# Kernel tuning notes

Hardware: AMD Instinct MI355X
Metric: run time of the kernel (lower is better)

Reference implementation:

```python
import jax, jax.numpy as jnp
import numpy as np
import math

EMBED_DIM = 1024
NUM_HEADS = 16
PROJ_DIM = 1024
HEAD_DIM = PROJ_DIM // NUM_HEADS  # 64
ALPHA = 0.3  # warmup_steps=0, step_count irrelevant -> alpha_eff = alpha
DIFFUSION_STEPS = 2


def setup_inputs() -> dict:
    key = jax.random.key(0)
    ks = jax.random.split(key, 9)
    B, N, D = 1, 2048, EMBED_DIM
    s_in = 1.0 / math.sqrt(D)
    s_p = 1.0 / math.sqrt(PROJ_DIM)
    return {
        "hidden_states": jax.random.normal(ks[0], (B, N, D), dtype=jnp.float32),
        # Linear weights stored as [in, out] (apply as x @ W + b)
        "Wq": jax.random.normal(ks[1], (D, PROJ_DIM), dtype=jnp.float32) * s_in,
        "bq": jax.random.normal(ks[2], (PROJ_DIM,), dtype=jnp.float32) * s_in,
        "Wk": jax.random.normal(ks[3], (D, PROJ_DIM), dtype=jnp.float32) * s_in,
        "bk": jax.random.normal(ks[4], (PROJ_DIM,), dtype=jnp.float32) * s_in,
        "Wv": jax.random.normal(ks[5], (D, PROJ_DIM), dtype=jnp.float32) * s_in,
        "bv": jax.random.normal(ks[6], (PROJ_DIM,), dtype=jnp.float32) * s_in,
        "Wo": jax.random.normal(ks[7], (PROJ_DIM, D), dtype=jnp.float32) * s_p,
        "bo": jax.random.normal(ks[8], (D,), dtype=jnp.float32) * s_p,
    }


def reference(hidden_states, Wq, bq, Wk, bk, Wv, bv, Wo, bo):
    B, N, D = hidden_states.shape
    H, hd = NUM_HEADS, HEAD_DIM

    def split_heads(x):  # [B, N, P] -> [B, H, N, hd]
        return x.reshape(B, -1, H, hd).transpose(0, 2, 1, 3)

    Q = split_heads(hidden_states @ Wq + bq)
    K = split_heads(hidden_states @ Wk + bk)
    V = split_heads(hidden_states @ Wv + bv)

    # scores: note original uses (sqrt(hd) + 1e-8) denominator here
    scores = jnp.einsum("bhqd,bhkd->bhqk", Q, K) / (math.sqrt(hd) + 1e-8)
    p0 = jax.nn.softmax(scores, axis=-1)

    # key-transition matrix P: exact sqrt(hd) denominator
    sim = jnp.einsum("bhid,bhjd->bhij", K, K) / math.sqrt(hd)
    P = jax.nn.softmax(sim, axis=-1)

    # iterative diffusion, unrolled (early-stop can only fire after the
    # final update when diffusion_steps=2, so output is identical)
    a = ALPHA
    p = p0
    for _ in range(DIFFUSION_STEPS):
        p = (1.0 - a) * p0 + a * jnp.einsum("bhqn,bhnm->bhqm", p, P)

    attn = jnp.einsum("bhqk,bhkd->bhqd", p, V)
    attn = attn.transpose(0, 2, 1, 3).reshape(B, N, PROJ_DIM)
    out = attn @ Wo + bo
    return out, p
```

## Files before the change

### kernel.cpp

```cpp
#include <hip/hip_runtime.h>


typedef __attribute__((ext_vector_type(8))) short bf16x8;
typedef __attribute__((ext_vector_type(4))) short s16x4;
typedef __attribute__((ext_vector_type(4))) float f32x4;

constexpr int N_TOK   = 2048;
constexpr int N_HEADS = 16;
constexpr int HD      = 64;
constexpr int EMB     = 1024;

#define DEVINL __device__ __forceinline__

DEVINL unsigned short f2bf_u(float f) {
  unsigned x = __float_as_uint(f);
  return (unsigned short)((x + 0x7fffu + ((x >> 16) & 1u)) >> 16);
}
DEVINL float bf2f_u(unsigned short h) { return __uint_as_float(((unsigned)h) << 16); }

DEVINL void async16(const void* src, void* dst) {
  __builtin_amdgcn_global_load_lds(
      (const __attribute__((address_space(1))) void*)src,
      (__attribute__((address_space(3))) void*)dst, 16, 0, 0);
}

enum : int { EPI_F32SCALE = 0, EPI_F32BIAS, EPI_BF16, EPI_QKSPLIT, EPI_VSPLIT,
             EPI_DIFF_BF16, EPI_DIFF_F32 };

template<int EPI>
__global__ __launch_bounds__(512, 2)
void gemm256_diff(const unsigned short* __restrict__ Am, int lda, long long sAz,
                  const unsigned short* __restrict__ Bm, int ldb, long long sBz,
                  int K,
                  const unsigned short* __restrict__ P0, int ldp0, long long sPz,
                  void* __restrict__ Cv, int ldc, long long sCz)
{
  __shared__ __align__(16) char smem[2 * 65536];
  const int tid  = threadIdx.x;
  const int lane = tid & 63, wv = tid >> 6;
  const int wr = wv >> 2, wc = wv & 3;
  const int l15 = lane & 15, g = lane >> 4;
  const int z = blockIdx.z;
  const size_t brow = (size_t)blockIdx.y * 256;
  const size_t bcol = (size_t)blockIdx.x * 256;

  const unsigned short* Ab = Am + (size_t)z * (size_t)sAz;
  const unsigned short* Bb = Bm + (size_t)z * (size_t)sBz;
  const int NT = K >> 6;

  const int cbs = (tid & 7) * 16;
  const int r00 = (tid >> 3),       r01 = 64  + (tid >> 3);
  const int r10 = 128 + (tid >> 3), r11 = 192 + (tid >> 3);
  const char* gA00 = (const char*)Ab + ((brow + r00) * (size_t)lda) * 2 + (cbs ^ ((r00 & 7) << 4));
  const char* gA01 = (const char*)Ab + ((brow + r01) * (size_t)lda) * 2 + (cbs ^ ((r01 & 7) << 4));
  const char* gA10 = (const char*)Ab + ((brow + r10) * (size_t)lda) * 2 + (cbs ^ ((r10 & 7) << 4));
  const char* gA11 = (const char*)Ab + ((brow + r11) * (size_t)lda) * 2 + (cbs ^ ((r11 & 7) << 4));
  const char* gB00 = (const char*)Bb + ((bcol + r00) * (size_t)ldb) * 2 + (cbs ^ ((r00 & 7) << 4));
  const char* gB01 = (const char*)Bb + ((bcol + r01) * (size_t)ldb) * 2 + (cbs ^ ((r01 & 7) << 4));
  const char* gB10 = (const char*)Bb + ((bcol + r10) * (size_t)ldb) * 2 + (cbs ^ ((r10 & 7) << 4));
  const char* gB11 = (const char*)Bb + ((bcol + r11) * (size_t)ldb) * 2 + (cbs ^ ((r11 & 7) << 4));

  f32x4 acc[8][4];
  #pragma unroll
  for (int m = 0; m < 8; ++m)
    #pragma unroll
    for (int n = 0; n < 4; ++n) acc[m][n] = f32x4{0.f, 0.f, 0.f, 0.f};

  auto ldA = [&](int cur, int mf, int kk) -> bf16x8 {
    const int row = wr * 128 + mf * 16 + l15;
    const int c = (kk * 64 + g * 16) ^ ((row & 7) << 4);
    return *(const bf16x8*)(smem + cur * 65536 + row * 128 + c);
  };
  auto ldB = [&](int cur, int nf, int kk) -> bf16x8 {
    const int row = wc * 64 + nf * 16 + l15;
    const int c = (kk * 64 + g * 16) ^ ((row & 7) << 4);
    return *(const bf16x8*)(smem + cur * 65536 + 32768 + row * 128 + c);
  };

  {
    char* d0 = smem;
    async16(gA00, d0 +             wv * 1024);
    async16(gA01, d0 +  8192 +     wv * 1024);
    async16(gA10, d0 + 16384 +     wv * 1024);
    async16(gA11, d0 + 24576 +     wv * 1024);
    async16(gB00, d0 + 32768 +     wv * 1024);
    async16(gB01, d0 + 40960 +     wv * 1024);
    async16(gB10, d0 + 49152 +     wv * 1024);
    async16(gB11, d0 + 57344 +     wv * 1024);
    if (NT > 1) {
      char* d1 = smem + 65536 + 32768;
      async16(gB00 + 128, d1 +             wv * 1024);
      async16(gB01 + 128, d1 +  8192 +     wv * 1024);
      async16(gB10 + 128, d1 + 16384 +     wv * 1024);
      async16(gB11 + 128, d1 + 24576 +     wv * 1024);
      asm volatile("s_waitcnt vmcnt(4)" ::: "memory");
    } else {
      asm volatile("s_waitcnt vmcnt(0)" ::: "memory");
    }
    __builtin_amdgcn_sched_barrier(0);
    __builtin_amdgcn_s_barrier();
  }

#define READA(P, Q)                                                       \
    bf16x8 P##00 = ldA(cur, 2*(Q),   0), P##01 = ldA(cur, 2*(Q),   1),    \
           P##10 = ldA(cur, 2*(Q)+1, 0), P##11 = ldA(cur, 2*(Q)+1, 1);

#define MFMA16(P, Q)                                                                        \
    __builtin_amdgcn_s_setprio(1);                                                          \
    acc[2*(Q)+0][0] = __builtin_amdgcn_mfma_f32_16x16x32_bf16(P##00, b00, acc[2*(Q)+0][0], 0, 0, 0); \
    acc[2*(Q)+0][1] = __builtin_amdgcn_mfma_f32_16x16x32_bf16(P##00, b10, acc[2*(Q)+0][1], 0, 0, 0); \
    acc[2*(Q)+0][2] = __builtin_amdgcn_mfma_f32_16x16x32_bf16(P##00, b20, acc[2*(Q)+0][2], 0, 0, 0); \
    acc[2*(Q)+0][3] = __builtin_amdgcn_mfma_f32_16x16x32_bf16(P##00, b30, acc[2*(Q)+0][3], 0, 0, 0); \
    acc[2*(Q)+1][0] = __builtin_amdgcn_mfma_f32_16x16x32_bf16(P##10, b00, acc[2*(Q)+1][0], 0, 0, 0); \
    acc[2*(Q)+1][1] = __builtin_amdgcn_mfma_f32_16x16x32_bf16(P##10, b10, acc[2*(Q)+1][1], 0, 0, 0); \
    acc[2*(Q)+1][2] = __builtin_amdgcn_mfma_f32_16x16x32_bf16(P##10, b20, acc[2*(Q)+1][2], 0, 0, 0); \
    acc[2*(Q)+1][3] = __builtin_amdgcn_mfma_f32_16x16x32_bf16(P##10, b30, acc[2*(Q)+1][3], 0, 0, 0); \
    acc[2*(Q)+0][0] = __builtin_amdgcn_mfma_f32_16x16x32_bf16(P##01, b01, acc[2*(Q)+0][0], 0, 0, 0); \
    acc[2*(Q)+0][1] = __builtin_amdgcn_mfma_f32_16x16x32_bf16(P##01, b11, acc[2*(Q)+0][1], 0, 0, 0); \
    acc[2*(Q)+0][2] = __builtin_amdgcn_mfma_f32_16x16x32_bf16(P##01, b21, acc[2*(Q)+0][2], 0, 0, 0); \
    acc[2*(Q)+0][3] = __builtin_amdgcn_mfma_f32_16x16x32_bf16(P##01, b31, acc[2*(Q)+0][3], 0, 0, 0); \
    acc[2*(Q)+1][0] = __builtin_amdgcn_mfma_f32_16x16x32_bf16(P##11, b01, acc[2*(Q)+1][0], 0, 0, 0); \
    acc[2*(Q)+1][1] = __builtin_amdgcn_mfma_f32_16x16x32_bf16(P##11, b11, acc[2*(Q)+1][1], 0, 0, 0); \
    acc[2*(Q)+1][2] = __builtin_amdgcn_mfma_f32_16x16x32_bf16(P##11, b21, acc[2*(Q)+1][2], 0, 0, 0); \
    acc[2*(Q)+1][3] = __builtin_amdgcn_mfma_f32_16x16x32_bf16(P##11, b31, acc[2*(Q)+1][3], 0, 0, 0); \
    __builtin_amdgcn_s_setprio(0);

#define SB __builtin_amdgcn_sched_barrier(0)

  int cur = 0;
  for (int t = 0; t < NT; ++t, cur ^= 1) {
    const int o = cur ^ 1;
    const size_t ko1 = (size_t)(t + 1) * 128;
    const size_t ko2 = (size_t)(t + 2) * 128;
    bf16x8 b00 = ldB(cur, 0, 0), b01 = ldB(cur, 0, 1);
    bf16x8 b10 = ldB(cur, 1, 0), b11 = ldB(cur, 1, 1);
    bf16x8 b20 = ldB(cur, 2, 0), b21 = ldB(cur, 2, 1);
    bf16x8 b30 = ldB(cur, 3, 0), b31 = ldB(cur, 3, 1);
    READA(f0_, 0)
    READA(f1_, 1)
    if (t + 1 < NT) {
      char* d = smem + o * 65536;
      async16(gA00 + ko1, d +        wv * 1024);
      async16(gA01 + ko1, d + 8192 + wv * 1024);
    }
    asm volatile("s_waitcnt lgkmcnt(4)" ::: "memory");
    SB;
    MFMA16(f0_, 0)
    READA(f2_, 2)
    if (t + 1 < NT) {
      char* d = smem + o * 65536;
      async16(gA10 + ko1, d + 16384 + wv * 1024);
      async16(gA11 + ko1, d + 24576 + wv * 1024);
    }
    asm volatile("s_waitcnt lgkmcnt(4)" ::: "memory");
    SB;
    MFMA16(f1_, 1)
    SB;
    __builtin_amdgcn_s_barrier();
    READA(f3_, 3)
    if (t + 2 < NT) {
      char* d = smem + cur * 65536 + 32768;
      async16(gB00 + ko2, d +        wv * 1024);
      async16(gB01 + ko2, d + 8192 + wv * 1024);
    }
    asm volatile("s_waitcnt lgkmcnt(4)" ::: "memory");
    SB;
    MFMA16(f2_, 2)
    if (t + 2 < NT) {
      char* d = smem + cur * 65536 + 32768 + 16384;
      async16(gB10 + ko2, d +        wv * 1024);
      async16(gB11 + ko2, d + 8192 + wv * 1024);
    }
    asm volatile("s_waitcnt lgkmcnt(0)" ::: "memory");
    SB;
    MFMA16(f3_, 3)
    if (t + 1 < NT) {
      if (t + 2 < NT) asm volatile("s_waitcnt vmcnt(4)" ::: "memory");
      else            asm volatile("s_waitcnt vmcnt(0)" ::: "memory");
      SB;
      __builtin_amdgcn_s_barrier();
    }
  }
#undef MFMA16
#undef READA
#undef SB

  float* Cf = (float*)Cv + (size_t)z * (size_t)sCz;
  unsigned short* Cu = (unsigned short*)Cv + (size_t)z * (size_t)sCz;
  const unsigned short* P0z = P0 + (size_t)z * (size_t)sPz;
  #pragma unroll
  for (int m = 0; m < 8; ++m)
  #pragma unroll
  for (int n = 0; n < 4; ++n)
  #pragma unroll
  for (int j = 0; j < 4; ++j) {
    const size_t R = brow + (size_t)(wr * 128 + m * 16 + g * 4 + j);
    const size_t C = bcol + (size_t)(wc * 64 + n * 16 + l15);
    const float v = acc[m][n][j];
    const float p0v = bf2f_u(P0z[R * (size_t)ldp0 + C]);
    const float r = 0.7f * p0v + 0.3f * v;
    if constexpr (EPI == EPI_DIFF_BF16) Cu[R * ldc + C] = f2bf_u(r);
    else                                Cf[R * ldc + C] = r;
  }
}

template<int BM, int BN, bool AF32, int EPI>
__global__ __launch_bounds__(256)
void gemm_tn(const void* __restrict__ Av, int lda, long long sAz,
             const unsigned short* __restrict__ Bm, int ldb, long long sBz,
             int K, float alpha, const float* __restrict__ bias,
             const unsigned short* __restrict__ P0, int ldp0, long long sPz,
             void* __restrict__ Cv, int ldc, long long sCz)
{
  constexpr int BKk = 64;
  constexpr int WM = BM / 2, WN = BN / 2, MF = WM / 16, NF = WN / 16;
  constexpr int AES = AF32 ? 4 : 2;
  constexpr int ABYTES = BM * BKk * AES, BBYTES = BN * BKk * 2;
  __shared__ __align__(16) char smem[ABYTES + BBYTES];

  const int tid  = threadIdx.x;
  const int lane = tid & 63, wv = tid >> 6;
  const int wr = wv >> 1, wc = wv & 1;
  const int l15 = lane & 15, g = lane >> 4;
  const int z = blockIdx.z;
  const size_t brow = (size_t)blockIdx.y * BM;
  const size_t bcol = (size_t)blockIdx.x * BN;

  const char* Ab = (const char*)Av + (size_t)z * (size_t)sAz * AES;
  const unsigned short* Bb = Bm + (size_t)z * (size_t)sBz;

  f32x4 acc[MF][NF];
  #pragma unroll
  for (int m = 0; m < MF; ++m)
    #pragma unroll
    for (int n = 0; n < NF; ++n)
      acc[m][n] = f32x4{0.f, 0.f, 0.f, 0.f};

  constexpr int EPC_A = AF32 ? 4 : 8;
  constexpr int CPR_A = BKk / EPC_A;
  constexpr int IT_A  = (BM * CPR_A) / 256;
  constexpr int CPR_B = 8;
  constexpr int IT_B  = (BN * CPR_B) / 256;

  for (int k0 = 0; k0 < K; k0 += BKk) {
    #pragma unroll
    for (int i = 0; i < IT_A; ++i) {
      const int c   = i * 256 + wv * 64 + lane;
      const int row = c / CPR_A;
      const int eo  = (c % CPR_A) * EPC_A;
      const char* src = Ab + ((brow + row) * (size_t)lda + (size_t)(k0 + eo)) * AES;
      async16(src, smem + (size_t)(i * 256 + wv * 64) * 16);
    }
    #pragma unroll
    for (int i = 0; i < IT_B; ++i) {
      const int c   = i * 256 + wv * 64 + lane;
      const int row = c / CPR_B;
      const int eo  = (c % CPR_B) * 8;
      const unsigned short* src = Bb + (bcol + row) * (size_t)ldb + (size_t)(k0 + eo);
      async16(src, smem + ABYTES + (size_t)(i * 256 + wv * 64) * 16);
    }
    __syncthreads();
    #pragma unroll
    for (int kk = 0; kk < 2; ++kk) {
      bf16x8 a[MF], b[NF];
      #pragma unroll
      for (int m = 0; m < MF; ++m) {
        const int r = wr * WM + m * 16 + l15;
        if constexpr (!AF32) {
          a[m] = *(const bf16x8*)(smem + ((size_t)r * BKk + kk * 32 + g * 8) * 2);
        } else {
          const float* pa = (const float*)smem + (size_t)r * BKk + kk * 32 + g * 8;
          const f32x4 lo = *(const f32x4*)pa;
          const f32x4 hi = *(const f32x4*)(pa + 4);
          bf16x8 t;
          t[0] = (short)f2bf_u(lo[0]); t[1] = (short)f2bf_u(lo[1]);
          t[2] = (short)f2bf_u(lo[2]); t[3] = (short)f2bf_u(lo[3]);
          t[4] = (short)f2bf_u(hi[0]); t[5] = (short)f2bf_u(hi[1]);
          t[6] = (short)f2bf_u(hi[2]); t[7] = (short)f2bf_u(hi[3]);
          a[m] = t;
        }
      }
      #pragma unroll
      for (int n = 0; n < NF; ++n) {
        const int cc = wc * WN + n * 16 + l15;
        b[n] = *(const bf16x8*)(smem + ABYTES + ((size_t)cc * BKk + kk * 32 + g * 8) * 2);
      }
      #pragma unroll
      for (int m = 0; m < MF; ++m)
        #pragma unroll
        for (int n = 0; n < NF; ++n)
          acc[m][n] = __builtin_amdgcn_mfma_f32_16x16x32_bf16(a[m], b[n], acc[m][n], 0, 0, 0);
    }
    __syncthreads();
  }

  float* Cf = (float*)Cv + (size_t)z * (size_t)sCz;
  unsigned short* Cu = (unsigned short*)Cv + (size_t)z * (size_t)sCz;

  #pragma unroll
  for (int m = 0; m < MF; ++m)
  #pragma unroll
  for (int n = 0; n < NF; ++n)
  #pragma unroll
  for (int j = 0; j < 4; ++j) {
    const size_t R  = brow + (size_t)(wr * WM + m * 16 + g * 4 + j);
    const size_t Cc = bcol + (size_t)(wc * WN + n * 16 + l15);
    const float v = acc[m][n][j];
    if constexpr (EPI == EPI_F32SCALE) {
      Cf[R * ldc + Cc] = v * alpha;
    } else if constexpr (EPI == EPI_F32BIAS) {
      Cf[R * ldc + Cc] = v + bias[Cc];
    } else if constexpr (EPI == EPI_BF16) {
      Cu[R * ldc + Cc] = f2bf_u(v);
    } else if constexpr (EPI == EPI_QKSPLIT) {
      const float t = v + bias[Cc];
      Cu[(Cc >> 6) * ((size_t)N_TOK * HD) + R * HD + (Cc & 63)] = f2bf_u(t);
    } else if constexpr (EPI == EPI_VSPLIT) {
      const float t = v + bias[Cc];
      Cu[(Cc >> 6) * ((size_t)HD * N_TOK) + (Cc & 63) * (size_t)N_TOK + R] = f2bf_u(t);
    } else if constexpr (EPI == EPI_DIFF_BF16) {
      const unsigned short* P0z = P0 + (size_t)z * (size_t)sPz;
      const float p0v = bf2f_u(P0z[R * (size_t)ldp0 + Cc]);
      Cu[R * ldc + Cc] = f2bf_u(0.7f * p0v + 0.3f * v);
    } else if constexpr (EPI == EPI_DIFF_F32) {
      const unsigned short* P0z = P0 + (size_t)z * (size_t)sPz;
      const float p0v = bf2f_u(P0z[R * (size_t)ldp0 + Cc]);
      Cf[R * ldc + Cc] = 0.7f * p0v + 0.3f * v;
    }
  }
  (void)alpha; (void)bias; (void)P0; (void)ldp0;
}

__global__ __launch_bounds__(256)
void row_softmax(const float* __restrict__ S, long long sS,
                 unsigned short* __restrict__ O, long long sO)
{
  __shared__ float red[8];
  const int tid = threadIdx.x;
  const size_t row = blockIdx.x;
  const size_t h = blockIdx.y;
  const f32x4* Sr = (const f32x4*)(S + (size_t)h * sS + row * N_TOK);
  f32x4 v0 = Sr[tid], v1 = Sr[tid + 256];
  float m = fmaxf(fmaxf(fmaxf(v0[0], v0[1]), fmaxf(v0[2], v0[3])),
                  fmaxf(fmaxf(v1[0], v1[1]), fmaxf(v1[2], v1[3])));
  #pragma unroll
  for (int o = 32; o; o >>= 1) m = fmaxf(m, __shfl_xor(m, o));
  if ((tid & 63) == 0) red[tid >> 6] = m;
  __syncthreads();
  m = fmaxf(fmaxf(red[0], red[1]), fmaxf(red[2], red[3]));
  f32x4 e0, e1;
  #pragma unroll
  for (int k = 0; k < 4; ++k) { e0[k] = expf(v0[k] - m); e1[k] = expf(v1[k] - m); }
  float s = e0[0]+e0[1]+e0[2]+e0[3]+e1[0]+e1[1]+e1[2]+e1[3];
  #pragma unroll
  for (int o = 32; o; o >>= 1) s += __shfl_xor(s, o);
  if ((tid & 63) == 0) red[4 + (tid >> 6)] = s;
  __syncthreads();
  s = red[4] + red[5] + red[6] + red[7];
  const float inv = 1.0f / s;
  s16x4 o0, o1;
  #pragma unroll
  for (int k = 0; k < 4; ++k) {
    o0[k] = (short)f2bf_u(e0[k] * inv);
    o1[k] = (short)f2bf_u(e1[k] * inv);
  }
  s16x4* Or = (s16x4*)(O + (size_t)h * sO + row * N_TOK);
  Or[tid] = o0; Or[tid + 256] = o1;
}

__global__ __launch_bounds__(256)
void row_reduce(const float* __restrict__ S, long long sS,
                float* __restrict__ mx, float* __restrict__ is_)
{
  __shared__ float red[8];
  const int tid = threadIdx.x;
  const size_t row = blockIdx.x;
  const size_t h = blockIdx.y;
  const f32x4* Sr = (const f32x4*)(S + (size_t)h * sS + row * N_TOK);
  f32x4 v0 = Sr[tid], v1 = Sr[tid + 256];
  float m = fmaxf(fmaxf(fmaxf(v0[0], v0[1]), fmaxf(v0[2], v0[3])),
                  fmaxf(fmaxf(v1[0], v1[1]), fmaxf(v1[2], v1[3])));
  #pragma unroll
  for (int o = 32; o; o >>= 1) m = fmaxf(m, __shfl_xor(m, o));
  if ((tid & 63) == 0) red[tid >> 6] = m;
  __syncthreads();
  m = fmaxf(fmaxf(red[0], red[1]), fmaxf(red[2], red[3]));
  float s = 0.f;
  #pragma unroll
  for (int k = 0; k < 4; ++k) { s += expf(v0[k] - m); s += expf(v1[k] - m); }
  #pragma unroll
  for (int o = 32; o; o >>= 1) s += __shfl_xor(s, o);
  if ((tid & 63) == 0) red[4 + (tid >> 6)] = s;
  __syncthreads();
  s = red[4] + red[5] + red[6] + red[7];
  if (tid == 0) { mx[h * N_TOK + row] = m; is_[h * N_TOK + row] = 1.0f / s; }
}

__global__ __launch_bounds__(256)
void pt_write(const float* __restrict__ S, long long sS,
              const float* __restrict__ mx, const float* __restrict__ is_,
              unsigned short* __restrict__ PT, long long sP)
{
  const int tid = threadIdx.x;
  const size_t row = blockIdx.x;
  const size_t h = blockIdx.y;
  const f32x4* Sr = (const f32x4*)(S + (size_t)h * sS + row * N_TOK);
  const f32x4* M4 = (const f32x4*)(mx + h * N_TOK);
  const f32x4* I4 = (const f32x4*)(is_ + h * N_TOK);
  s16x4* Pr = (s16x4*)(PT + (size_t)h * sP + row * N_TOK);
  #pragma unroll
  for (int i = 0; i < 2; ++i) {
    const int idx = tid + i * 256;
    f32x4 sv = Sr[idx], mv = M4[idx], iv = I4[idx];
    s16x4 o;
    #pragma unroll
    for (int k = 0; k < 4; ++k) o[k] = (short)f2bf_u(expf(sv[k] - mv[k]) * iv[k]);
    Pr[idx] = o;
  }
}

__global__ __launch_bounds__(256)
void transpose_cast4(const float* __restrict__ w0, const float* __restrict__ w1,
                     const float* __restrict__ w2, const float* __restrict__ w3,
                     unsigned short* __restrict__ o0, unsigned short* __restrict__ o1,
                     unsigned short* __restrict__ o2, unsigned short* __restrict__ o3)
{
  __shared__ float tile[64][65];
  const float* in; unsigned short* out;
  if      (blockIdx.z == 0) { in = w0; out = o0; }
  else if (blockIdx.z == 1) { in = w1; out = o1; }
  else if (blockIdx.z == 2) { in = w2; out = o2; }
  else                      { in = w3; out = o3; }
  const int n = EMB;
  const int bx = blockIdx.x * 64, by = blockIdx.y * 64;
  const int tid = threadIdx.x;
  const int r = tid >> 2;
  const int q = tid & 3;
  #pragma unroll
  for (int i = 0; i < 4; ++i) {
    const int c = q * 16 + i * 4;
    f32x4 v = *(const f32x4*)(in + (size_t)(by + r) * n + bx + c);
    tile[r][c + 0] = v[0]; tile[r][c + 1] = v[1];
    tile[r][c + 2] = v[2]; tile[r][c + 3] = v[3];
  }
  __syncthreads();
  #pragma unroll
  for (int i = 0; i < 4; ++i) {
    const int c0 = q * 16 + i * 4;
    s16x4 o;
    o[0] = (short)f2bf_u(tile[c0 + 0][r]); o[1] = (short)f2bf_u(tile[c0 + 1][r]);
    o[2] = (short)f2bf_u(tile[c0 + 2][r]); o[3] = (short)f2bf_u(tile[c0 + 3][r]);
    *(s16x4*)(out + (size_t)(bx + r) * n + by + c0) = o;
  }
}

__global__ __launch_bounds__(256)
void cast_f32_bf16(const float* __restrict__ in, unsigned short* __restrict__ out)
{
  const size_t i = (size_t)blockIdx.x * 256 + threadIdx.x;
  f32x4 v = ((const f32x4*)in)[i];
  s16x4 o;
  o[0] = (short)f2bf_u(v[0]); o[1] = (short)f2bf_u(v[1]);
  o[2] = (short)f2bf_u(v[2]); o[3] = (short)f2bf_u(v[3]);
  ((s16x4*)out)[i] = o;
}

extern "C" void kernel_launch(void* const* d_in, const int* in_sizes, int n_in,
                              void* d_out, int out_size, void* d_ws, size_t ws_size,
                              hipStream_t stream)
{
  (void)in_sizes; (void)n_in; (void)out_size;
  const float* hs = (const float*)d_in[0];
  const float* Wq = (const float*)d_in[1];
  const float* bq = (const float*)d_in[2];
  const float* Wk = (const float*)d_in[3];
  const float* bk = (const float*)d_in[4];
  const float* Wv = (const float*)d_in[5];
  const float* bv = (const float*)d_in[6];
  const float* Wo = (const float*)d_in[7];
  const float* bo = (const float*)d_in[8];

  float* outO = (float*)d_out;
  float* outP = outO + (size_t)N_TOK * EMB;

  const long long NN = (long long)N_TOK * N_TOK;

  const bool batched = ws_size >= ((size_t)440 << 20);
  const int PH = batched ? N_HEADS : 1;

  char* ws = (char*)d_ws;
  auto alloc = [&](size_t b) { char* p = ws; ws += (b + 255) & ~(size_t)255; return p; };
  unsigned short* Xbf = (unsigned short*)alloc((size_t)N_TOK * EMB * 2);
  unsigned short* WqT = (unsigned short*)alloc((size_t)EMB * EMB * 2);
  unsigned short* WkT = (unsigned short*)alloc((size_t)EMB * EMB * 2);
  unsigned short* WvT = (unsigned short*)alloc((size_t)EMB * EMB * 2);
  unsigned short* WoT = (unsigned short*)alloc((size_t)EMB * EMB * 2);
  unsigned short* Qb  = (unsigned short*)alloc((size_t)N_HEADS * N_TOK * HD * 2);
  unsigned short* Kb  = (unsigned short*)alloc((size_t)N_HEADS * N_TOK * HD * 2);
  unsigned short* Vt  = (unsigned short*)alloc((size_t)N_HEADS * N_TOK * HD * 2);
  unsigned short* attn= (unsigned short*)alloc((size_t)N_TOK * EMB * 2);
  float* mx  = (float*)alloc((size_t)PH * N_TOK * 4);
  float* is_ = (float*)alloc((size_t)PH * N_TOK * 4);
  unsigned short* p0b = (unsigned short*)alloc((size_t)PH * NN * 2);
  unsigned short* PT  = (unsigned short*)alloc((size_t)PH * NN * 2);
  unsigned short* p1b = (unsigned short*)alloc((size_t)PH * NN * 2);

  cast_f32_bf16<<<dim3(N_TOK * EMB / 1024), 256, 0, stream>>>(hs, Xbf);
  transpose_cast4<<<dim3(16, 16, 4), 256, 0, stream>>>(Wq, Wk, Wv, Wo, WqT, WkT, WvT, WoT);

  gemm_tn<128, 128, false, EPI_QKSPLIT><<<dim3(EMB / 128, N_TOK / 128, 1), 256, 0, stream>>>(
      Xbf, EMB, 0, WqT, EMB, 0, EMB, 0.f, bq, nullptr, 0, 0, Qb, 0, 0);
  gemm_tn<128, 128, false, EPI_QKSPLIT><<<dim3(EMB / 128, N_TOK / 128, 1), 256, 0, stream>>>(
      Xbf, EMB, 0, WkT, EMB, 0, EMB, 0.f, bk, nullptr, 0, 0, Kb, 0, 0);
  gemm_tn<128, 128, false, EPI_VSPLIT><<<dim3(EMB / 128, N_TOK / 128, 1), 256, 0, stream>>>(
      Xbf, EMB, 0, WvT, EMB, 0, EMB, 0.f, bv, nullptr, 0, 0, Vt, 0, 0);

  if (batched) {
    const long long sH = (long long)N_TOK * HD;
    gemm_tn<128, 128, false, EPI_F32SCALE><<<dim3(16, 16, N_HEADS), 256, 0, stream>>>(
        Qb, HD, sH, Kb, HD, sH, HD, 0.125f, nullptr, nullptr, 0, 0, outP, N_TOK, NN);
    row_softmax<<<dim3(N_TOK, N_HEADS), 256, 0, stream>>>(outP, NN, p0b, NN);
    gemm_tn<128, 128, false, EPI_F32SCALE><<<dim3(16, 16, N_HEADS), 256, 0, stream>>>(
        Kb, HD, sH, Kb, HD, sH, HD, 0.125f, nullptr, nullptr, 0, 0, outP, N_TOK, NN);
    row_reduce<<<dim3(N_TOK, N_HEADS), 256, 0, stream>>>(outP, NN, mx, is_);
    pt_write<<<dim3(N_TOK, N_HEADS), 256, 0, stream>>>(outP, NN, mx, is_, PT, NN);
    gemm256_diff<EPI_DIFF_BF16><<<dim3(8, 8, N_HEADS), 512, 0, stream>>>(
        p0b, N_TOK, NN, PT, N_TOK, NN, N_TOK, p0b, N_TOK, NN, p1b, N_TOK, NN);
    gemm256_diff<EPI_DIFF_F32><<<dim3(8, 8, N_HEADS), 512, 0, stream>>>(
        p1b, N_TOK, NN, PT, N_TOK, NN, N_TOK, p0b, N_TOK, NN, outP, N_TOK, NN);
    gemm_tn<128, 64, true, EPI_BF16><<<dim3(1, N_TOK / 128, N_HEADS), 256, 0, stream>>>(
        outP, N_TOK, NN, Vt, N_TOK, (long long)HD * N_TOK,
        N_TOK, 0.f, nullptr, nullptr, 0, 0, attn, EMB, HD);
  } else {
    for (int h = 0; h < N_HEADS; ++h) {
      float* slot = outP + (size_t)h * NN;
      const unsigned short* Qh = Qb + (size_t)h * N_TOK * HD;
      const unsigned short* Kh = Kb + (size_t)h * N_TOK * HD;
      gemm_tn<128, 128, false, EPI_F32SCALE><<<dim3(16, 16, 1), 256, 0, stream>>>(
          Qh, HD, 0, Kh, HD, 0, HD, 0.125f, nullptr, nullptr, 0, 0, slot, N_TOK, 0);
      row_softmax<<<dim3(N_TOK, 1), 256, 0, stream>>>(slot, 0, p0b, 0);
      gemm_tn<128, 128, false, EPI_F32SCALE><<<dim3(16, 16, 1), 256, 0, stream>>>(
          Kh, HD, 0, Kh, HD, 0, HD, 0.125f, nullptr, nullptr, 0, 0, slot, N_TOK, 0);
      row_reduce<<<dim3(N_TOK, 1), 256, 0, stream>>>(slot, 0, mx, is_);
      pt_write<<<dim3(N_TOK, 1), 256, 0, stream>>>(slot, 0, mx, is_, PT, 0);
      gemm_tn<128, 128, false, EPI_DIFF_BF16><<<dim3(16, 16, 1), 256, 0, stream>>>(
          p0b, N_TOK, 0, PT, N_TOK, 0, N_TOK, 0.f, nullptr, p0b, N_TOK, 0, p1b, N_TOK, 0);
      gemm_tn<128, 128, false, EPI_DIFF_F32><<<dim3(16, 16, 1), 256, 0, stream>>>(
          p1b, N_TOK, 0, PT, N_TOK, 0, N_TOK, 0.f, nullptr, p0b, N_TOK, 0, slot, N_TOK, 0);
    }
    gemm_tn<128, 64, true, EPI_BF16><<<dim3(1, N_TOK / 128, N_HEADS), 256, 0, stream>>>(
        outP, N_TOK, NN, Vt, N_TOK, (long long)HD * N_TOK,
        N_TOK, 0.f, nullptr, nullptr, 0, 0, attn, EMB, HD);
  }

  gemm_tn<128, 128, false, EPI_F32BIAS><<<dim3(EMB / 128, N_TOK / 128, 1), 256, 0, stream>>>(
      attn, EMB, 0, WoT, EMB, 0, EMB, 0.f, bo, nullptr, 0, 0, outO, EMB, 0);
}
```

Measured before the change: 1.052 ms.

## Compute softmax stats by recomputing QK^T and fuse normalization into GEMM epilogue

Adds a gemm_stats kernel that recomputes the score rows with MFMA and keeps an online max and sum-of-exp per row, then fuses the softmax normalization into the score GEMM epilogue (row-wise for p0, column-wise for the transposed P). This removes writing and re-reading the full fp32 score matrices through global memory and drops the separate softmax, reduce and transpose-write kernels. In exchange the K=64 score GEMM is computed twice and the epilogue does more exp work.

```diff
diff --git a/kernel.cpp b/kernel.cpp
--- a/kernel.cpp
+++ b/kernel.cpp
@@ -25,7 +25,128 @@
 }
 
 enum : int { EPI_F32SCALE = 0, EPI_F32BIAS, EPI_BF16, EPI_QKSPLIT, EPI_VSPLIT,
-             EPI_DIFF_BF16, EPI_DIFF_F32 };
+             EPI_DIFF_BF16, EPI_DIFF_F32, EPI_SM_ROW, EPI_SM_COL };
+
+__global__ __launch_bounds__(256)
+void gemm_stats(const unsigned short* __restrict__ Am, long long sAz,
+                const unsigned short* __restrict__ Bm, long long sBz,
+                float alpha, float* __restrict__ mxo, float* __restrict__ iso)
+{
+  __shared__ __align__(16) char smem[3 * 16384];
+  __shared__ float lred[2][2][128];
+  const int tid = threadIdx.x, lane = tid & 63, wv = tid >> 6;
+  const int wr = wv >> 1, wc = wv & 1, l15 = lane & 15, g = lane >> 4;
+  const size_t z = blockIdx.y;
+  const unsigned short* Az = Am + z * (size_t)sAz + (size_t)blockIdx.x * 128 * HD;
+  const unsigned short* Bz = Bm + z * (size_t)sBz;
+  const int cbs = (tid & 7) * 16;
+  const int rr = tid >> 3;
+
+  #pragma unroll
+  for (int i = 0; i < 4; ++i) {
+    const int r = i * 32 + rr;
+    async16((const char*)Az + (size_t)r * 128 + (cbs ^ ((r & 7) << 4)),
+            smem + i * 4096 + wv * 1024);
+  }
+  #pragma unroll
+  for (int i = 0; i < 4; ++i) {
+    const int r = i * 32 + rr;
+    async16((const char*)Bz + (size_t)r * 128 + (cbs ^ ((r & 7) << 4)),
+            smem + 16384 + i * 4096 + wv * 1024);
+  }
+  __syncthreads();
+
+  float rm[4][4], rs[4][4];
+  #pragma unroll
+  for (int m = 0; m < 4; ++m)
+    #pragma unroll
+    for (int j = 0; j < 4; ++j) { rm[m][j] = -3.0e38f; rs[m][j] = 0.f; }
+
+  for (int ct = 0; ct < 16; ++ct) {
+    const int cur = ct & 1;
+    if (ct + 1 < 16) {
+      const int nb = cur ^ 1;
+      #pragma unroll
+      for (int i = 0; i < 4; ++i) {
+        const int r = i * 32 + rr;
+        const size_t br = (size_t)(ct + 1) * 128 + r;
+        async16((const char*)Bz + br * 128 + (cbs ^ ((r & 7) << 4)),
+                smem + 16384 + nb * 16384 + i * 4096 + wv * 1024);
+      }
+    }
+    f32x4 acc[4][4];
+    #pragma unroll
+    for (int m = 0; m < 4; ++m)
+      #pragma unroll
+      for (int n = 0; n < 4; ++n) acc[m][n] = f32x4{0.f, 0.f, 0.f, 0.f};
+    #pragma unroll
+    for (int kk = 0; kk < 2; ++kk) {
+      bf16x8 a[4], b[4];
+      #pragma unroll
+      for (int m = 0; m < 4; ++m) {
+        const int row = wr * 64 + m * 16 + l15;
+        const int c = (kk * 64 + g * 16) ^ ((row & 7) << 4);
+        a[m] = *(const bf16x8*)(smem + row * 128 + c);
+      }
+      #pragma unroll
+      for (int n = 0; n < 4; ++n) {
+        const int row = wc * 64 + n * 16 + l15;
+        const int c = (kk * 64 + g * 16) ^ ((row & 7) << 4);
+        b[n] = *(const bf16x8*)(smem + 16384 + cur * 16384 + row * 128 + c);
+      }
+      #pragma unroll
+      for (int m = 0; m < 4; ++m)
+        #pragma unroll
+        for (int n = 0; n < 4; ++n)
+          acc[m][n] = __builtin_amdgcn_mfma_f32_16x16x32_bf16(a[m], b[n], acc[m][n], 0, 0, 0);
+    }
+    #pragma unroll
+    for (int m = 0; m < 4; ++m)
+    #pragma unroll
+    for (int j = 0; j < 4; ++j) {
+      const float v0 = acc[m][0][j] * alpha, v1 = acc[m][1][j] * alpha;
+      const float v2 = acc[m][2][j] * alpha, v3 = acc[m][3][j] * alpha;
+      const float pm = fmaxf(fmaxf(v0, v1), fmaxf(v2, v3));
+      const float nm = fmaxf(rm[m][j], pm);
+      rs[m][j] = rs[m][j] * expf(rm[m][j] - nm)
+               + expf(v0 - nm) + expf(v1 - nm) + expf(v2 - nm) + expf(v3 - nm);
+      rm[m][j] = nm;
+    }
+    __syncthreads();
+  }
+
+  #pragma unroll
+  for (int off = 1; off < 16; off <<= 1) {
+    #pragma unroll
+    for (int m = 0; m < 4; ++m)
+    #pragma unroll
+    for (int j = 0; j < 4; ++j) {
+      const float om = __shfl_xor(rm[m][j], off);
+      const float os = __shfl_xor(rs[m][j], off);
+      const float nm = fmaxf(rm[m][j], om);
+      rs[m][j] = rs[m][j] * expf(rm[m][j] - nm) + os * expf(om - nm);
+      rm[m][j] = nm;
+    }
+  }
+  if (l15 == 0) {
+    #pragma unroll
+    for (int m = 0; m < 4; ++m)
+    #pragma unroll
+    for (int j = 0; j < 4; ++j) {
+      const int r = wr * 64 + m * 16 + g * 4 + j;
+      lred[0][wc][r] = rm[m][j];
+      lred[1][wc][r] = rs[m][j];
+    }
+  }
+  __syncthreads();
+  if (tid < 128) {
+    const float m0 = lred[0][0][tid], m1 = lred[0][1][tid];
+    const float M = fmaxf(m0, m1);
+    const float S = lred[1][0][tid] * expf(m0 - M) + lred[1][1][tid] * expf(m1 - M);
+    mxo[z * N_TOK + (size_t)blockIdx.x * 128 + tid] = M;
+    iso[z * N_TOK + (size_t)blockIdx.x * 128 + tid] = 1.0f / S;
+  }
+}
 
 template<int EPI>
 __global__ __launch_bounds__(512, 2)
@@ -209,6 +330,7 @@
 void gemm_tn(const void* __restrict__ Av, int lda, long long sAz,
              const unsigned short* __restrict__ Bm, int ldb, long long sBz,
              int K, float alpha, const float* __restrict__ bias,
+             const float* __restrict__ mxp, const float* __restrict__ isp,
              const unsigned short* __restrict__ P0, int ldp0, long long sPz,
              void* __restrict__ Cv, int ldc, long long sCz)
 {
@@ -326,9 +448,17 @@
       const unsigned short* P0z = P0 + (size_t)z * (size_t)sPz;
       const float p0v = bf2f_u(P0z[R * (size_t)ldp0 + Cc]);
       Cf[R * ldc + Cc] = 0.7f * p0v + 0.3f * v;
-    }
-  }
-  (void)alpha; (void)bias; (void)P0; (void)ldp0;
+    } else if constexpr (EPI == EPI_SM_ROW) {
+      const float M = mxp[(size_t)z * N_TOK + R];
+      const float S = isp[(size_t)z * N_TOK + R];
+      Cu[R * ldc + Cc] = f2bf_u(expf(v * alpha - M) * S);
+    } else if constexpr (EPI == EPI_SM_COL) {
+      const float M = mxp[(size_t)z * N_TOK + Cc];
+      const float S = isp[(size_t)z * N_TOK + Cc];
+      Cu[R * ldc + Cc] = f2bf_u(expf(v * alpha - M) * S);
+    }
+  }
+  (void)alpha; (void)bias; (void)mxp; (void)isp; (void)P0; (void)ldp0;
 }
 
 __global__ __launch_bounds__(256)
@@ -484,6 +614,7 @@
   float* outP = outO + (size_t)N_TOK * EMB;
 
   const long long NN = (long long)N_TOK * N_TOK;
+  const long long sH = (long long)N_TOK * HD;
 
   const bool batched = ws_size >= ((size_t)440 << 20);
   const int PH = batched ? N_HEADS : 1;
@@ -499,8 +630,10 @@
   unsigned short* Kb  = (unsigned short*)alloc((size_t)N_HEADS * N_TOK * HD * 2);
   unsigned short* Vt  = (unsigned short*)alloc((size_t)N_HEADS * N_TOK * HD * 2);
   unsigned short* attn= (unsigned short*)alloc((size_t)N_TOK * EMB * 2);
-  float* mx  = (float*)alloc((size_t)PH * N_TOK * 4);
-  float* is_ = (float*)alloc((size_t)PH * N_TOK * 4);
+  float* mxq = (float*)alloc((size_t)N_HEADS * N_TOK * 4);
+  float* isq = (float*)alloc((size_t)N_HEADS * N_TOK * 4);
+  float* mxk = (float*)alloc((size_t)N_HEADS * N_TOK * 4);
+  float* isk = (float*)alloc((size_t)N_HEADS * N_TOK * 4);
   unsigned short* p0b = (unsigned short*)alloc((size_t)PH * NN * 2);
   unsigned short* PT  = (unsigned short*)alloc((size_t)PH * NN * 2);
   unsigned short* p1b = (unsigned short*)alloc((size_t)PH * NN * 2);
@@ -509,50 +642,48 @@
   transpose_cast4<<<dim3(16, 16, 4), 256, 0, stream>>>(Wq, Wk, Wv, Wo, WqT, WkT, WvT, WoT);
 
   gemm_tn<128, 128, false, EPI_QKSPLIT><<<dim3(EMB / 128, N_TOK / 128, 1), 256, 0, stream>>>(
-      Xbf, EMB, 0, WqT, EMB, 0, EMB, 0.f, bq, nullptr, 0, 0, Qb, 0, 0);
+      Xbf, EMB, 0, WqT, EMB, 0, EMB, 0.f, bq, nullptr, nullptr, nullptr, 0, 0, Qb, 0, 0);
   gemm_tn<128, 128, false, EPI_QKSPLIT><<<dim3(EMB / 128, N_TOK / 128, 1), 256, 0, stream>>>(
-      Xbf, EMB, 0, WkT, EMB, 0, EMB, 0.f, bk, nullptr, 0, 0, Kb, 0, 0);
+      Xbf, EMB, 0, WkT, EMB, 0, EMB, 0.f, bk, nullptr, nullptr, nullptr, 0, 0, Kb, 0, 0);
   gemm_tn<128, 128, false, EPI_VSPLIT><<<dim3(EMB / 128, N_TOK / 128, 1), 256, 0, stream>>>(
-      Xbf, EMB, 0, WvT, EMB, 0, EMB, 0.f, bv, nullptr, 0, 0, Vt, 0, 0);
+      Xbf, EMB, 0, WvT, EMB, 0, EMB, 0.f, bv, nullptr, nullptr, nullptr, 0, 0, Vt, 0, 0);
 
   if (batched) {
-    const long long sH = (long long)N_TOK * HD;
-    gemm_tn<128, 128, false, EPI_F32SCALE><<<dim3(16, 16, N_HEADS), 256, 0, stream>>>(
-        Qb, HD, sH, Kb, HD, sH, HD, 0.125f, nullptr, nullptr, 0, 0, outP, N_TOK, NN);
-    row_softmax<<<dim3(N_TOK, N_HEADS), 256, 0, stream>>>(outP, NN, p0b, NN);
-    gemm_tn<128, 128, false, EPI_F32SCALE><<<dim3(16, 16, N_HEADS), 256, 0, stream>>>(
-        Kb, HD, sH, Kb, HD, sH, HD, 0.125f, nullptr, nullptr, 0, 0, outP, N_TOK, NN);
-    row_reduce<<<dim3(N_TOK, N_HEADS), 256, 0, stream>>>(outP, NN, mx, is_);
-    pt_write<<<dim3(N_TOK, N_HEADS), 256, 0, stream>>>(outP, NN, mx, is_, PT, NN);
+    gemm_stats<<<dim3(16, N_HEADS), 256, 0, stream>>>(Qb, sH, Kb, sH, 0.125f, mxq, isq);
+    gemm_tn<128, 128, false, EPI_SM_ROW><<<dim3(16, 16, N_HEADS), 256, 0, stream>>>(
+        Qb, HD, sH, Kb, HD, sH, HD, 0.125f, nullptr, mxq, isq, nullptr, 0, 0, p0b, N_TOK, NN);
+    gemm_stats<<<dim3(16, N_HEADS), 256, 0, stream>>>(Kb, sH, Kb, sH, 0.125f, mxk, isk);
+    gemm_tn<128, 128, false, EPI_SM_COL><<<dim3(16, 16, N_HEADS), 256, 0, stream>>>(
+        Kb, HD, sH, Kb, HD, sH, HD, 0.125f, nullptr, mxk, isk, nullptr, 0, 0, PT, N_TOK, NN);
     gemm256_diff<EPI_DIFF_BF16><<<dim3(8, 8, N_HEADS), 512, 0, stream>>>(
         p0b, N_TOK, NN, PT, N_TOK, NN, N_TOK, p0b, N_TOK, NN, p1b, N_TOK, NN);
     gemm256_diff<EPI_DIFF_F32><<<dim3(8, 8, N_HEADS), 512, 0, stream>>>(
         p1b, N_TOK, NN, PT, N_TOK, NN, N_TOK, p0b, N_TOK, NN, outP, N_TOK, NN);
     gemm_tn<128, 64, true, EPI_BF16><<<dim3(1, N_TOK / 128, N_HEADS), 256, 0, stream>>>(
         outP, N_TOK, NN, Vt, N_TOK, (long long)HD * N_TOK,
-        N_TOK, 0.f, nullptr, nullptr, 0, 0, attn, EMB, HD);
+        N_TOK, 0.f, nullptr, nullptr, nullptr, nullptr, 0, 0, attn, EMB, HD);
   } else {
     for (int h = 0; h < N_HEADS; ++h) {
       float* slot = outP + (size_t)h * NN;
       const unsigned short* Qh = Qb + (size_t)h * N_TOK * HD;
       const unsigned short* Kh = Kb + (size_t)h * N_TOK * HD;
       gemm_tn<128, 128, false, EPI_F32SCALE><<<dim3(16, 16, 1), 256, 0, stream>>>(
-          Qh, HD, 0, Kh, HD, 0, HD, 0.125f, nullptr, nullptr, 0, 0, slot, N_TOK, 0);
+          Qh, HD, 0, Kh, HD, 0, HD, 0.125f, nullptr, nullptr, nullptr, nullptr, 0, 0, slot, N_TOK, 0);
       row_softmax<<<dim3(N_TOK, 1), 256, 0, stream>>>(slot, 0, p0b, 0);
       gemm_tn<128, 128, false, EPI_F32SCALE><<<dim3(16, 16, 1), 256, 0, stream>>>(
-          Kh, HD, 0, Kh, HD, 0, HD, 0.125f, nullptr, nullptr, 0, 0, slot, N_TOK, 0);
-      row_reduce<<<dim3(N_TOK, 1), 256, 0, stream>>>(slot, 0, mx, is_);
-      pt_write<<<dim3(N_TOK, 1), 256, 0, stream>>>(slot, 0, mx, is_, PT, 0);
+          Kh, HD, 0, Kh, HD, 0, HD, 0.125f, nullptr, nullptr, nullptr, nullptr, 0, 0, slot, N_TOK, 0);
+      row_reduce<<<dim3(N_TOK, 1), 256, 0, stream>>>(slot, 0, mxq, isq);
+      pt_write<<<dim3(N_TOK, 1), 256, 0, stream>>>(slot, 0, mxq, isq, PT, 0);
       gemm_tn<128, 128, false, EPI_DIFF_BF16><<<dim3(16, 16, 1), 256, 0, stream>>>(
-          p0b, N_TOK, 0, PT, N_TOK, 0, N_TOK, 0.f, nullptr, p0b, N_TOK, 0, p1b, N_TOK, 0);
+          p0b, N_TOK, 0, PT, N_TOK, 0, N_TOK, 0.f, nullptr, nullptr, nullptr, p0b, N_TOK, 0, p1b, N_TOK, 0);
       gemm_tn<128, 128, false, EPI_DIFF_F32><<<dim3(16, 16, 1), 256, 0, stream>>>(
-          p1b, N_TOK, 0, PT, N_TOK, 0, N_TOK, 0.f, nullptr, p0b, N_TOK, 0, slot, N_TOK, 0);
+          p1b, N_TOK, 0, PT, N_TOK, 0, N_TOK, 0.f, nullptr, nullptr, nullptr, p0b, N_TOK, 0, slot, N_TOK, 0);
     }
     gemm_tn<128, 64, true, EPI_BF16><<<dim3(1, N_TOK / 128, N_HEADS), 256, 0, stream>>>(
         outP, N_TOK, NN, Vt, N_TOK, (long long)HD * N_TOK,
-        N_TOK, 0.f, nullptr, nullptr, 0, 0, attn, EMB, HD);
+        N_TOK, 0.f, nullptr, nullptr, nullptr, nullptr, 0, 0, attn, EMB, HD);
   }
 
   gemm_tn<128, 128, false, EPI_F32BIAS><<<dim3(EMB / 128, N_TOK / 128, 1), 256, 0, stream>>>(
-      attn, EMB, 0, WoT, EMB, 0, EMB, 0.f, bo, nullptr, 0, 0, outO, EMB, 0);
-}
+      attn, EMB, 0, WoT, EMB, 0, EMB, 0.f, bo, nullptr, nullptr, nullptr, 0, 0, outO, EMB, 0);
+}
```

After: 975.2 us. 7.3% less time.
